# Kernel tuning notes

Measured on AMD Instinct MI355X. Metric: run time of the kernel, lower is better.

## Reference

```python
import jax, jax.numpy as jnp
import numpy as np

IN_FEATURES = 4096
OUT_FEATURES = 4096
ALPHA = 0.002
BETA = 0.01


def setup_inputs() -> dict:
    key = jax.random.key(0)
    k_x, k_w, k_b = jax.random.split(key, 3)
    # int8 activations, weights, bias (matching torch.randint(-127, 127, ...))
    x = jax.random.randint(k_x, (4, 2048, IN_FEATURES), -127, 127, dtype=jnp.int32).astype(jnp.int8)
    weight = jax.random.randint(k_w, (OUT_FEATURES, IN_FEATURES), -127, 127, dtype=jnp.int32).astype(jnp.int8)
    bias = jax.random.randint(k_b, (1, OUT_FEATURES), -127, 127, dtype=jnp.int32).astype(jnp.int8)
    a = jnp.float32(ALPHA)
    b = jnp.float32(BETA)
    return {"x": x, "weight": weight, "bias": bias, "a": a, "b": b}


def reference(x, weight, bias, a, b):
    # int8 bias add, and requantize-to-int8 epilogue.
    x_shape = x.shape
    x2d = x.reshape(-1, x_shape[-1])                       # [M, K] int8
    # int32 accumulation: acc = x @ W^T
    acc = jnp.matmul(x2d.astype(jnp.int32), weight.T.astype(jnp.int32),
                     preferred_element_type=jnp.int32)      # [M, N] int32
    # epilogue: alpha * acc + beta * bias, round + clamp to int8 range
    y = a * acc.astype(jnp.float32) + b * bias.astype(jnp.float32)
    y = jnp.clip(jnp.round(y), -128.0, 127.0).astype(jnp.int8)
    return y.reshape(*x_shape[:-1], -1)
```

## Files before the change

kernel.cpp:

```cpp
#include <hip/hip_runtime.h>

#define K_DIM 4096
#define N_DIM 4096
#define NT (K_DIM / 64)

typedef int v4i __attribute__((ext_vector_type(4)));

__device__ __forceinline__ void gload_lds16(const void* g, void* l) {
  __builtin_amdgcn_global_load_lds(
      (const __attribute__((address_space(1))) void*)g,
      (__attribute__((address_space(3))) void*)l, 16, 0, 0);
}

__device__ __forceinline__ int pack4(int4 w) {
  return (w.x & 0xff) | ((w.y & 0xff) << 8) | ((w.z & 0xff) << 16) | (w.w << 24);
}

__global__ __launch_bounds__(256) void pack_kernel(const int* __restrict__ x,
                                                   const int* __restrict__ w,
                                                   int4* __restrict__ dst, int n16x,
                                                   int n16) {
  int i = blockIdx.x * 256 + threadIdx.x;
  if (i >= n16) return;
  const int4* s = (i < n16x) ? ((const int4*)x + (size_t)i * 4)
                             : ((const int4*)w + (size_t)(i - n16x) * 4);
  int4 w0 = s[0], w1 = s[1], w2 = s[2], w3 = s[3];
  int4 r;
  r.x = pack4(w0); r.y = pack4(w1); r.z = pack4(w2); r.w = pack4(w3);
  dst[i] = r;
}

__global__ __launch_bounds__(512, 2) void gemm256(
    const char* __restrict__ Ap, const char* __restrict__ Bp,
    const int* __restrict__ bias, const float* __restrict__ pa,
    const float* __restrict__ pb, int* __restrict__ out) {
  extern __shared__ __align__(16) char lds[];

  const int tid = threadIdx.x;
  const int wid = tid >> 6;
  const int lane = tid & 63;

  const int nwg = gridDim.x;
  const int cpx = nwg >> 3;
  const int flat = blockIdx.x;
  const int wg = (flat & 7) * cpx + (flat >> 3);
  const int br = wg >> 4;
  const int bn = wg & 15;

  const int wr = wid >> 2;
  const int wcol = wid & 3;

  const int srow = tid >> 2;
  const int schunk = (tid & 3) ^ ((tid >> 3) & 3);
  const char* aSrc = Ap + (size_t)(br * 256 + srow) * K_DIM + schunk * 16;
  const char* bSrc = Bp + (size_t)(bn * 256 + srow) * K_DIM + schunk * 16;

  auto stage = [&](int kt) {
    const char* sa = aSrc + kt * 64;
    const char* sb2 = bSrc + kt * 64;
    char* da = lds + (kt & 3) * 16384 + wid * 1024;
    char* db = lds + 65536 + (kt & 3) * 16384 + wid * 1024;
    gload_lds16(sa, da);
    gload_lds16(sa + (size_t)128 * K_DIM, da + 8192);
    gload_lds16(sb2, db);
    gload_lds16(sb2 + (size_t)128 * K_DIM, db + 8192);
  };

  const int lrow = lane & 15;
  const int fchunk = lane >> 4;
  const int rchunk = fchunk ^ ((lrow >> 1) & 3);
  const int aOff = (wr * 128 + lrow) * 64 + rchunk * 16;
  const int bOff = 65536 + (wcol * 64 + lrow) * 64 + rchunk * 16;

  v4i acc[8][4];
  {
    v4i z = {0, 0, 0, 0};
#pragma unroll
    for (int mi = 0; mi < 8; ++mi)
#pragma unroll
      for (int ni = 0; ni < 4; ++ni) acc[mi][ni] = z;
  }

  stage(0); stage(1); stage(2);
  asm volatile("s_waitcnt vmcnt(8)" ::: "memory");
  __builtin_amdgcn_s_barrier();

  for (int kt = 0; kt < NT; ++kt) {
    const int sb = (kt & 3) * 16384;

    v4i bf[4], af[8];
#pragma unroll
    for (int ni = 0; ni < 4; ++ni) bf[ni] = *(const v4i*)&lds[sb + bOff + ni * 1024];
    af[0] = *(const v4i*)&lds[sb + aOff + 0 * 1024];
    af[1] = *(const v4i*)&lds[sb + aOff + 1 * 1024];
    if (kt + 3 < NT) stage(kt + 3);
    __builtin_amdgcn_sched_barrier(0);

#pragma unroll
    for (int mi = 0; mi < 8; ++mi) {
      if (mi + 2 < 8) af[mi + 2] = *(const v4i*)&lds[sb + aOff + (mi + 2) * 1024];
      __builtin_amdgcn_sched_barrier(0);
      __builtin_amdgcn_s_setprio(1);
#pragma unroll
      for (int ni = 0; ni < 4; ++ni)
        acc[mi][ni] =
            __builtin_amdgcn_mfma_i32_16x16x64_i8(af[mi], bf[ni], acc[mi][ni], 0, 0, 0);
      __builtin_amdgcn_s_setprio(0);
      __builtin_amdgcn_sched_barrier(0);
    }

    if (kt < NT - 3)
      asm volatile("s_waitcnt vmcnt(4)" ::: "memory");
    else
      asm volatile("s_waitcnt vmcnt(0)" ::: "memory");
    __builtin_amdgcn_s_barrier();
  }

  const float alpha = *pa;
  const float beta = *pb;
  const int rg = lane >> 4;
#pragma unroll
  for (int ni = 0; ni < 4; ++ni) {
    const int n = bn * 256 + wcol * 64 + ni * 16 + lrow;
    const float bb2 = __fmul_rn(beta, (float)bias[n]);
#pragma unroll
    for (int mi = 0; mi < 8; ++mi) {
#pragma unroll
      for (int j = 0; j < 4; ++j) {
        const int m = br * 256 + wr * 128 + mi * 16 + rg * 4 + j;
        float y = __fadd_rn(__fmul_rn(alpha, (float)acc[mi][ni][j]), bb2);
        y = rintf(y);
        y = fminf(127.f, fmaxf(-128.f, y));
        out[(size_t)m * N_DIM + n] = (int)y;
      }
    }
  }
}

extern "C" void kernel_launch(void* const* d_in, const int* in_sizes, int n_in,
                              void* d_out, int out_size, void* d_ws, size_t ws_size,
                              hipStream_t stream) {
  const int* x = (const int*)d_in[0];
  const int* w = (const int*)d_in[1];
  const int* bias = (const int*)d_in[2];
  const float* pa = (const float*)d_in[3];
  const float* pb = (const float*)d_in[4];
  int* out = (int*)d_out;

  const int M = in_sizes[0] / K_DIM;
  const size_t xBytes = (size_t)M * K_DIM;
  const size_t wBytes = (size_t)N_DIM * K_DIM;

  char* xp = (char*)d_ws;
  char* wp = xp + xBytes;
  const int n16x = (int)(xBytes / 16);
  const int n16 = (int)((xBytes + wBytes) / 16);
  pack_kernel<<<(n16 + 255) / 256, 256, 0, stream>>>(x, (const int*)d_in[1],
                                                     (int4*)xp, n16x, n16);

  const int nwg = (M / 256) * (N_DIM / 256);
  hipFuncSetAttribute((const void*)gemm256,
                      hipFuncAttributeMaxDynamicSharedMemorySize, 131072);
  gemm256<<<nwg, 512, 131072, stream>>>(xp, wp, bias, pa, pb, out);
}
```

Before: 195.0 us.

## Use 4 waves per block with 128x128 per-wave tiles in int8 GEMM

Reshapes the 256x256 block from 8 waves (128x64 each) to 4 waves (128x128 each), doubling the accumulator count per wave to 64 v4i. Each thread now issues eight LDS-direct loads per stage, and the wait counts are adjusted to match. The larger per-wave tile raises register reuse of A and B fragments, and setprio is removed. This risks heavy VGPR/AGPR pressure with 256 accumulator registers and fewer waves available to hide latency.

```diff
diff --git a/kernel.cpp b/kernel.cpp
--- a/kernel.cpp
+++ b/kernel.cpp
@@ -30,7 +30,7 @@
   dst[i] = r;
 }
 
-__global__ __launch_bounds__(512, 2) void gemm256(
+__global__ __launch_bounds__(256, 1) void gemm256(
     const char* __restrict__ Ap, const char* __restrict__ Bp,
     const int* __restrict__ bias, const float* __restrict__ pa,
     const float* __restrict__ pb, int* __restrict__ out) {
@@ -47,8 +47,8 @@
   const int br = wg >> 4;
   const int bn = wg & 15;
 
-  const int wr = wid >> 2;
-  const int wcol = wid & 3;
+  const int wr = wid >> 1;
+  const int wc = wid & 1;
 
   const int srow = tid >> 2;
   const int schunk = (tid & 3) ^ ((tid >> 3) & 3);
@@ -56,61 +56,61 @@
   const char* bSrc = Bp + (size_t)(bn * 256 + srow) * K_DIM + schunk * 16;
 
   auto stage = [&](int kt) {
+    const int s = (kt & 3) * 16384;
     const char* sa = aSrc + kt * 64;
     const char* sb2 = bSrc + kt * 64;
-    char* da = lds + (kt & 3) * 16384 + wid * 1024;
-    char* db = lds + 65536 + (kt & 3) * 16384 + wid * 1024;
-    gload_lds16(sa, da);
-    gload_lds16(sa + (size_t)128 * K_DIM, da + 8192);
-    gload_lds16(sb2, db);
-    gload_lds16(sb2 + (size_t)128 * K_DIM, db + 8192);
+    char* da = lds + s + tid * 16;
+    char* db = lds + 65536 + s + tid * 16;
+#pragma unroll
+    for (int j = 0; j < 4; ++j) {
+      gload_lds16(sa + (size_t)j * 64 * K_DIM, da + j * 4096);
+      gload_lds16(sb2 + (size_t)j * 64 * K_DIM, db + j * 4096);
+    }
   };
 
   const int lrow = lane & 15;
   const int fchunk = lane >> 4;
   const int rchunk = fchunk ^ ((lrow >> 1) & 3);
   const int aOff = (wr * 128 + lrow) * 64 + rchunk * 16;
-  const int bOff = 65536 + (wcol * 64 + lrow) * 64 + rchunk * 16;
+  const int bOff = 65536 + (wc * 128 + lrow) * 64 + rchunk * 16;
 
-  v4i acc[8][4];
+  v4i acc[8][8];
   {
     v4i z = {0, 0, 0, 0};
 #pragma unroll
     for (int mi = 0; mi < 8; ++mi)
 #pragma unroll
-      for (int ni = 0; ni < 4; ++ni) acc[mi][ni] = z;
+      for (int ni = 0; ni < 8; ++ni) acc[mi][ni] = z;
   }
 
   stage(0); stage(1); stage(2);
-  asm volatile("s_waitcnt vmcnt(8)" ::: "memory");
+  asm volatile("s_waitcnt vmcnt(16)" ::: "memory");
   __builtin_amdgcn_s_barrier();
 
   for (int kt = 0; kt < NT; ++kt) {
     const int sb = (kt & 3) * 16384;
 
-    v4i bf[4], af[8];
+    v4i af[8], bf[8];
 #pragma unroll
-    for (int ni = 0; ni < 4; ++ni) bf[ni] = *(const v4i*)&lds[sb + bOff + ni * 1024];
-    af[0] = *(const v4i*)&lds[sb + aOff + 0 * 1024];
-    af[1] = *(const v4i*)&lds[sb + aOff + 1 * 1024];
+    for (int mi = 0; mi < 8; ++mi) af[mi] = *(const v4i*)&lds[sb + aOff + mi * 1024];
+    bf[0] = *(const v4i*)&lds[sb + bOff + 0 * 1024];
+    bf[1] = *(const v4i*)&lds[sb + bOff + 1 * 1024];
     if (kt + 3 < NT) stage(kt + 3);
     __builtin_amdgcn_sched_barrier(0);
 
 #pragma unroll
-    for (int mi = 0; mi < 8; ++mi) {
-      if (mi + 2 < 8) af[mi + 2] = *(const v4i*)&lds[sb + aOff + (mi + 2) * 1024];
+    for (int ni = 0; ni < 8; ++ni) {
+      if (ni + 2 < 8) bf[ni + 2] = *(const v4i*)&lds[sb + bOff + (ni + 2) * 1024];
       __builtin_amdgcn_sched_barrier(0);
-      __builtin_amdgcn_s_setprio(1);
 #pragma unroll
-      for (int ni = 0; ni < 4; ++ni)
+      for (int mi = 0; mi < 8; ++mi)
         acc[mi][ni] =
             __builtin_amdgcn_mfma_i32_16x16x64_i8(af[mi], bf[ni], acc[mi][ni], 0, 0, 0);
-      __builtin_amdgcn_s_setprio(0);
       __builtin_amdgcn_sched_barrier(0);
     }
 
-    if (kt < NT - 3)
-      asm volatile("s_waitcnt vmcnt(4)" ::: "memory");
+    if (kt + 3 < NT)
+      asm volatile("s_waitcnt vmcnt(8)" ::: "memory");
     else
       asm volatile("s_waitcnt vmcnt(0)" ::: "memory");
     __builtin_amdgcn_s_barrier();
@@ -120,8 +120,8 @@
   const float beta = *pb;
   const int rg = lane >> 4;
 #pragma unroll
-  for (int ni = 0; ni < 4; ++ni) {
-    const int n = bn * 256 + wcol * 64 + ni * 16 + lrow;
+  for (int ni = 0; ni < 8; ++ni) {
+    const int n = bn * 256 + wc * 128 + ni * 16 + lrow;
     const float bb2 = __fmul_rn(beta, (float)bias[n]);
 #pragma unroll
     for (int mi = 0; mi < 8; ++mi) {
@@ -161,5 +161,5 @@
   const int nwg = (M / 256) * (N_DIM / 256);
   hipFuncSetAttribute((const void*)gemm256,
                       hipFuncAttributeMaxDynamicSharedMemorySize, 131072);
-  gemm256<<<nwg, 512, 131072, stream>>>(xp, wp, bias, pa, pb, out);
+  gemm256<<<nwg, 256, 131072, stream>>>(xp, wp, bias, pa, pb, out);
 }
```

New measurement: 214.4 us. +9.9%, slower.

## Split K-step into two barrier-separated MFMA phases with staggered A/B prefetch

Applied to the files above, without the earlier changes.

Restructures the main GEMM loop into two half-steps, each loading four A fragments and running 16 MFMAs between workgroup barriers. The global-to-LDS prefetch for A is issued in the first phase and for B in the second, so memory issue is spread out and interleaved with compute in a ping-pong style. The vmcnt waits are retuned to match the split. It also changes the LDS destination addressing to tid*16. The added barriers per iteration may cost synchronization overhead, and the coarser waits reduce fine-grained overlap of LDS reads with MFMAs.

```diff
diff --git a/kernel.cpp b/kernel.cpp
--- a/kernel.cpp
+++ b/kernel.cpp
@@ -55,15 +55,19 @@
   const char* aSrc = Ap + (size_t)(br * 256 + srow) * K_DIM + schunk * 16;
   const char* bSrc = Bp + (size_t)(bn * 256 + srow) * K_DIM + schunk * 16;
 
-  auto stage = [&](int kt) {
+  auto stageA = [&](int kt) {
+    const int s = (kt & 3) * 16384;
     const char* sa = aSrc + kt * 64;
-    const char* sb2 = bSrc + kt * 64;
-    char* da = lds + (kt & 3) * 16384 + wid * 1024;
-    char* db = lds + 65536 + (kt & 3) * 16384 + wid * 1024;
+    char* da = lds + s + tid * 16;
     gload_lds16(sa, da);
     gload_lds16(sa + (size_t)128 * K_DIM, da + 8192);
-    gload_lds16(sb2, db);
-    gload_lds16(sb2 + (size_t)128 * K_DIM, db + 8192);
+  };
+  auto stageB = [&](int kt) {
+    const int s = (kt & 3) * 16384;
+    const char* sbp = bSrc + kt * 64;
+    char* db = lds + 65536 + s + tid * 16;
+    gload_lds16(sbp, db);
+    gload_lds16(sbp + (size_t)128 * K_DIM, db + 8192);
   };
 
   const int lrow = lane & 15;
@@ -81,38 +85,55 @@
       for (int ni = 0; ni < 4; ++ni) acc[mi][ni] = z;
   }
 
-  stage(0); stage(1); stage(2);
+  stageA(0); stageB(0);
+  stageA(1); stageB(1);
+  stageA(2); stageB(2);
   asm volatile("s_waitcnt vmcnt(8)" ::: "memory");
   __builtin_amdgcn_s_barrier();
 
   for (int kt = 0; kt < NT; ++kt) {
     const int sb = (kt & 3) * 16384;
+    v4i af[4], bf[4];
 
-    v4i bf[4], af[8];
+#pragma unroll
+    for (int mi = 0; mi < 4; ++mi) af[mi] = *(const v4i*)&lds[sb + aOff + mi * 1024];
 #pragma unroll
     for (int ni = 0; ni < 4; ++ni) bf[ni] = *(const v4i*)&lds[sb + bOff + ni * 1024];
-    af[0] = *(const v4i*)&lds[sb + aOff + 0 * 1024];
-    af[1] = *(const v4i*)&lds[sb + aOff + 1 * 1024];
-    if (kt + 3 < NT) stage(kt + 3);
+    if (kt + 3 < NT) stageA(kt + 3);
+    __builtin_amdgcn_s_barrier();
+    asm volatile("s_waitcnt lgkmcnt(0)" ::: "memory");
     __builtin_amdgcn_sched_barrier(0);
-
+    __builtin_amdgcn_s_setprio(1);
 #pragma unroll
-    for (int mi = 0; mi < 8; ++mi) {
-      if (mi + 2 < 8) af[mi + 2] = *(const v4i*)&lds[sb + aOff + (mi + 2) * 1024];
-      __builtin_amdgcn_sched_barrier(0);
-      __builtin_amdgcn_s_setprio(1);
+    for (int mi = 0; mi < 4; ++mi)
 #pragma unroll
       for (int ni = 0; ni < 4; ++ni)
         acc[mi][ni] =
             __builtin_amdgcn_mfma_i32_16x16x64_i8(af[mi], bf[ni], acc[mi][ni], 0, 0, 0);
-      __builtin_amdgcn_s_setprio(0);
-      __builtin_amdgcn_sched_barrier(0);
-    }
+    __builtin_amdgcn_s_setprio(0);
+    __builtin_amdgcn_s_barrier();
 
+#pragma unroll
+    for (int mi = 0; mi < 4; ++mi)
+      af[mi] = *(const v4i*)&lds[sb + aOff + (mi + 4) * 1024];
+    if (kt + 3 < NT) stageB(kt + 3);
     if (kt < NT - 3)
+      asm volatile("s_waitcnt vmcnt(8)" ::: "memory");
+    else if (kt == NT - 3)
       asm volatile("s_waitcnt vmcnt(4)" ::: "memory");
     else
       asm volatile("s_waitcnt vmcnt(0)" ::: "memory");
+    __builtin_amdgcn_s_barrier();
+    asm volatile("s_waitcnt lgkmcnt(0)" ::: "memory");
+    __builtin_amdgcn_sched_barrier(0);
+    __builtin_amdgcn_s_setprio(1);
+#pragma unroll
+    for (int mi = 0; mi < 4; ++mi)
+#pragma unroll
+      for (int ni = 0; ni < 4; ++ni)
+        acc[mi + 4][ni] =
+            __builtin_amdgcn_mfma_i32_16x16x64_i8(af[mi], bf[ni], acc[mi + 4][ni], 0, 0, 0);
+    __builtin_amdgcn_s_setprio(0);
     __builtin_amdgcn_s_barrier();
   }
 
```

After: 197.4 us. No clear change (+1.2%).

## Prefetch next k-tile LDS fragments during current MFMAs with register double-buffering

Applied to the files above, without the earlier changes.

Restructures the main loop so the A and B fragments for the next k-tile are read from LDS while the MFMAs for the current tile run. Two ping-pong register sets replace the per-iteration reload, and the loop is unrolled by two. The prologue now waits for two stages before the first fragment loads. This hides LDS read latency behind MFMA work, at the cost of more VGPRs (afA, afB and bf held together) and an extra lgkmcnt wait before each barrier, which could hurt occupancy under the two-workgroup launch bound.

```diff
diff --git a/kernel.cpp b/kernel.cpp
--- a/kernel.cpp
+++ b/kernel.cpp
@@ -56,10 +56,11 @@
   const char* bSrc = Bp + (size_t)(bn * 256 + srow) * K_DIM + schunk * 16;
 
   auto stage = [&](int kt) {
+    const int s = (kt & 3) * 16384;
     const char* sa = aSrc + kt * 64;
     const char* sb2 = bSrc + kt * 64;
-    char* da = lds + (kt & 3) * 16384 + wid * 1024;
-    char* db = lds + 65536 + (kt & 3) * 16384 + wid * 1024;
+    char* da = lds + s + wid * 1024;
+    char* db = lds + 65536 + s + wid * 1024;
     gload_lds16(sa, da);
     gload_lds16(sa + (size_t)128 * K_DIM, da + 8192);
     gload_lds16(sb2, db);
@@ -81,40 +82,48 @@
       for (int ni = 0; ni < 4; ++ni) acc[mi][ni] = z;
   }
 
+  v4i afA[8], afB[8], bf[4];
+
   stage(0); stage(1); stage(2);
-  asm volatile("s_waitcnt vmcnt(8)" ::: "memory");
+  asm volatile("s_waitcnt vmcnt(4)" ::: "memory");
   __builtin_amdgcn_s_barrier();
+#pragma unroll
+  for (int mi = 0; mi < 8; ++mi) afA[mi] = *(const v4i*)&lds[aOff + mi * 1024];
+#pragma unroll
+  for (int ni = 0; ni < 4; ++ni) bf[ni] = *(const v4i*)&lds[bOff + ni * 1024];
 
-  for (int kt = 0; kt < NT; ++kt) {
-    const int sb = (kt & 3) * 16384;
+#define INTERVAL(KT, AFC, AFN)                                                       \
+  do {                                                                               \
+    const int sbn = (((KT) + 1) & 3) * 16384;                                        \
+    if ((KT) + 3 < NT) stage((KT) + 3);                                              \
+    __builtin_amdgcn_sched_barrier(0);                                               \
+    _Pragma("unroll") for (int mi = 0; mi < 8; ++mi) {                               \
+      if ((KT) + 1 < NT) AFN[mi] = *(const v4i*)&lds[sbn + aOff + mi * 1024];        \
+      __builtin_amdgcn_sched_barrier(0);                                             \
+      __builtin_amdgcn_s_setprio(1);                                                 \
+      _Pragma("unroll") for (int ni = 0; ni < 4; ++ni)                               \
+          acc[mi][ni] = __builtin_amdgcn_mfma_i32_16x16x64_i8(AFC[mi], bf[ni],       \
+                                                              acc[mi][ni], 0, 0, 0); \
+      __builtin_amdgcn_s_setprio(0);                                                 \
+      __builtin_amdgcn_sched_barrier(0);                                             \
+    }                                                                                \
+    if ((KT) + 1 < NT) {                                                             \
+      _Pragma("unroll") for (int ni = 0; ni < 4; ++ni)                               \
+          bf[ni] = *(const v4i*)&lds[sbn + bOff + ni * 1024];                        \
+    }                                                                                \
+    if ((KT) < NT - 3)                                                               \
+      asm volatile("s_waitcnt vmcnt(4)" ::: "memory");                               \
+    else                                                                             \
+      asm volatile("s_waitcnt vmcnt(0)" ::: "memory");                               \
+    asm volatile("s_waitcnt lgkmcnt(0)" ::: "memory");                               \
+    __builtin_amdgcn_s_barrier();                                                    \
+  } while (0)
 
-    v4i bf[4], af[8];
-#pragma unroll
-    for (int ni = 0; ni < 4; ++ni) bf[ni] = *(const v4i*)&lds[sb + bOff + ni * 1024];
-    af[0] = *(const v4i*)&lds[sb + aOff + 0 * 1024];
-    af[1] = *(const v4i*)&lds[sb + aOff + 1 * 1024];
-    if (kt + 3 < NT) stage(kt + 3);
-    __builtin_amdgcn_sched_barrier(0);
-
-#pragma unroll
-    for (int mi = 0; mi < 8; ++mi) {
-      if (mi + 2 < 8) af[mi + 2] = *(const v4i*)&lds[sb + aOff + (mi + 2) * 1024];
-      __builtin_amdgcn_sched_barrier(0);
-      __builtin_amdgcn_s_setprio(1);
-#pragma unroll
-      for (int ni = 0; ni < 4; ++ni)
-        acc[mi][ni] =
-            __builtin_amdgcn_mfma_i32_16x16x64_i8(af[mi], bf[ni], acc[mi][ni], 0, 0, 0);
-      __builtin_amdgcn_s_setprio(0);
-      __builtin_amdgcn_sched_barrier(0);
-    }
-
-    if (kt < NT - 3)
-      asm volatile("s_waitcnt vmcnt(4)" ::: "memory");
-    else
-      asm volatile("s_waitcnt vmcnt(0)" ::: "memory");
-    __builtin_amdgcn_s_barrier();
+  for (int kt = 0; kt < NT; kt += 2) {
+    INTERVAL(kt, afA, afB);
+    INTERVAL(kt + 1, afB, afA);
   }
+#undef INTERVAL
 
   const float alpha = *pa;
   const float beta = *pb;
```

Result: no change. 195.5 us (+0.2%).
